# Kernel tuning notes

Measured on AMD Instinct MI355X. Metric: run time of the kernel, lower is better.

## Reference

```python
import jax, jax.numpy as jnp
import numpy as np


def setup_inputs() -> dict:
    key = jax.random.key(0)
    k1, k2 = jax.random.split(key)
    template = jax.random.normal(k1, (5, 8, 2), dtype=jnp.float32)        # (R, A, 2)
    projections = jax.random.normal(k2, (5000, 8, 2), dtype=jnp.float32)  # (V, K0, 2)
    return {"template": template, "projections": projections}


def _compute_bc(template, projections):
    # template: (R, A, 2); projections: (V, K0, 2)
    R, A = template.shape[:2]
    V, K0 = projections.shape[:2]
    K = K0 - 1  # number of 'other' (non-closest) neighbors

    # --- nearest-neighbor ordering of projected neighbors per template vertex ---
    diff = template[None, :, :, None, :] - projections[:, None, None, :, :]   # (V,R,A,K0,2)
    order = jnp.argsort(jnp.linalg.norm(diff, axis=-1), axis=-1)              # (V,R,A,K0)
    gathered = jnp.take_along_axis(projections[:, None, None, :, :], order[..., None], axis=3)  # (V,R,A,K0,2)
    closest = gathered[..., 0, :]   # (V,R,A,2)
    other = gathered[..., 1:, :]    # (V,R,A,K,2)

    # --- barycentric weights for every candidate (second, third) vertex pair ---
    # v0 == v1 in the original code (both other - closest)
    v0 = other - closest[..., None, :]          # (V,R,A,K,2)
    v2 = template[None] - closest               # (V,R,A,2)
    dot00 = jnp.einsum('vrani,vrani->vran', v0, v0)      # == dot11
    dot01 = jnp.einsum('vrani,vrami->vranm', v0, v0)
    dot02 = jnp.einsum('vrani,vrai->vran', v0, v2)       # == dot12

    eye = jnp.eye(K, dtype=bool)
    denom = dot00[..., :, None] * dot00[..., None, :] - dot01 * dot01   # (V,R,A,K,K)
    # original zeroes the diagonal then takes 1/0 = inf; we use a safe value and
    # explicitly invalidate the diagonal below (identical final output).
    inv = 1.0 / jnp.where(eye, 1.0, denom)
    w2 = (dot00[..., None, :] * dot02[..., :, None] - dot01 * dot02[..., None, :]) * inv
    w1 = (dot00[..., :, None] * dot02[..., None, :] - dot01 * dot02[..., :, None]) * inv
    w0 = 1.0 - w2 - w1
    weights = jnp.stack([w0, w2, w1], axis=-1)           # (V,R,A,K,K,3)

    invalid = (weights <= 0.0) | jnp.isnan(weights) | eye[:, :, None]
    weights = jnp.where(invalid, jnp.inf, weights)
    score = jnp.max(weights * weights, axis=-1)          # inf-norm of squared weights, (V,R,A,K,K)

    # --- Delaunay (empty-circumcircle) condition, dense over all (n, m, j) ---
    s_all = jnp.sum(gathered * gathered, axis=-1)        # x^2 + y^2, (V,R,A,K0)
    sc, so = s_all[..., 0], s_all[..., 1:]
    cx, cy = closest[..., 0], closest[..., 1]
    ox, oy = other[..., 0], other[..., 1]
    # rows of 4x4 incircle matrix: [closest, other[n], other[m], other[j]] with
    # columns [x, y, x^2+y^2, 1]; reduce rows by subtracting row 4 -> 3x3 det.
    ax = cx[..., None, None, None] - ox[..., None, None, :]   # (V,R,A,1,1,K)
    ay = cy[..., None, None, None] - oy[..., None, None, :]
    as_ = sc[..., None, None, None] - so[..., None, None, :]
    bx = ox[..., :, None, None] - ox[..., None, None, :]      # (V,R,A,K,1,K)
    by = oy[..., :, None, None] - oy[..., None, None, :]
    bs = so[..., :, None, None] - so[..., None, None, :]
    dx = ox[..., None, :, None] - ox[..., None, None, :]      # (V,R,A,1,K,K)
    dy = oy[..., None, :, None] - oy[..., None, None, :]
    ds = so[..., None, :, None] - so[..., None, None, :]
    det = ax * (by * ds - bs * dy) - ay * (bx * ds - bs * dx) + as_ * (bx * dy - by * dx)  # (V,R,A,K,K,K)
    j_is_tri = eye[:, None, :] | eye[None, :, :]              # exclude j == n or j == m
    ok = jnp.all((det <= 0.0) | j_is_tri, axis=-1)            # (V,R,A,K,K)
    score = jnp.where(ok, score, jnp.inf)

    # --- select best (second, third) pair per template vertex ---
    flat = score.reshape(V, R, A, K * K)
    idx = jnp.argmin(flat, axis=-1)                            # (V,R,A)
    row, col = idx // K, idx % K
    wf = weights.reshape(V, R, A, K * K, 3)
    w_sel = jnp.take_along_axis(wf, idx[..., None, None], axis=3)[..., 0, :]  # (V,R,A,3)
    zero_mask = jnp.any(jnp.isinf(w_sel), axis=-1, keepdims=True)
    w_sel = jnp.where(zero_mask, 0.0, w_sel)

    oh = order[..., 1:]                                        # (V,R,A,K)
    nbr_idx = jnp.take_along_axis(oh, jnp.stack([row, col], axis=-1), axis=-1)  # (V,R,A,2)
    indices = jnp.concatenate([order[..., :1], nbr_idx], axis=-1).astype(jnp.int32)  # (V,R,A,3)
    return w_sel, indices


def reference(template, projections):
    return _compute_bc(template, projections)
```

## Files before the change

### kernel.cpp

```cpp
#include <hip/hip_runtime.h>
#include <math.h>

#define R_DIM 5
#define A_DIM 8
#define K0    8
#define KK    7
#define NPAIR 21

#define PID(p, q) ((p) * 7 - (p) * ((p) + 1) / 2 + ((q) - (p) - 1))

__global__ __launch_bounds__(256) void bc_kernel(
    const float* __restrict__ tmpl,
    const float* __restrict__ proj,
    float* __restrict__ out,
    int ntask)
{
#pragma clang fp contract(off)
    const float INF = __builtin_inff();
    int tid = blockIdx.x * blockDim.x + threadIdx.x;
    if (tid >= ntask) return;
    int v  = tid / (R_DIM * A_DIM);
    int ra = tid - v * (R_DIM * A_DIM);

    float tx = tmpl[ra * 2 + 0];
    float ty = tmpl[ra * 2 + 1];

    const float4* pv4 = reinterpret_cast<const float4*>(proj + (size_t)v * (K0 * 2));
    float4 q0 = pv4[0], q1 = pv4[1], q2 = pv4[2], q3 = pv4[3];
    float px[K0] = {q0.x, q0.z, q1.x, q1.z, q2.x, q2.z, q3.x, q3.z};
    float py[K0] = {q0.y, q0.w, q1.y, q1.w, q2.y, q2.w, q3.y, q3.w};
    float ps[K0], pd[K0];
#pragma unroll
    for (int k = 0; k < K0; ++k) {
        ps[k] = px[k] * px[k] + py[k] * py[k];
        float dx = tx - px[k], dy = ty - py[k];
        pd[k] = sqrtf(dx * dx + dy * dy);
    }

    int rank[K0];
#pragma unroll
    for (int k = 0; k < K0; ++k) {
        int r = 0;
#pragma unroll
        for (int l = 0; l < K0; ++l)
            r += (pd[l] < pd[k] || (pd[l] == pd[k] && l < k)) ? 1 : 0;
        rank[k] = r;
    }

    float cx = 0.f, cy = 0.f, cs = 0.f; int cidx = 0;
#pragma unroll
    for (int k = 0; k < K0; ++k) {
        bool h = (rank[k] == 0);
        cx = h ? px[k] : cx;  cy = h ? py[k] : cy;
        cs = h ? ps[k] : cs;  cidx = h ? k : cidx;
    }

    float ox[KK], oy[KK], osq[KK]; int ork[KK], oid[KK];
#pragma unroll
    for (int n = 0; n < KK; ++n) {
        bool ge = (n >= cidx);
        ox[n]  = ge ? px[n + 1]   : px[n];
        oy[n]  = ge ? py[n + 1]   : py[n];
        osq[n] = ge ? ps[n + 1]   : ps[n];
        ork[n] = ge ? rank[n + 1] : rank[n];
        oid[n] = ge ? (n + 1)     : n;
    }

    float v2x = tx - cx, v2y = ty - cy;
    float vx[KK], vy[KK], d00[KK], d02[KK];
#pragma unroll
    for (int n = 0; n < KK; ++n) {
        vx[n] = ox[n] - cx;
        vy[n] = oy[n] - cy;
        d00[n] = vx[n] * vx[n] + vy[n] * vy[n];
        d02[n] = vx[n] * v2x + vy[n] * v2y;
    }

    float dmn[NPAIR], dmx[NPAIR];
#pragma unroll
    for (int i = 0; i < NPAIR; ++i) { dmn[i] = INF; dmx[i] = -INF; }

#pragma unroll
    for (int k = 0; k < KK; ++k) {
        float akx = cx - ox[k], aky = cy - oy[k], aks = cs - osq[k];
        float ex[KK], ey[KK], es[KK];
#pragma unroll
        for (int i = 0; i < KK; ++i) {
            if (i == k) continue;
            ex[i] = ox[i] - ox[k];
            ey[i] = oy[i] - oy[k];
            es[i] = osq[i] - osq[k];
        }
#pragma unroll
        for (int p = 0; p < KK - 1; ++p) {
#pragma unroll
            for (int q = p + 1; q < KK; ++q) {
                if (p == k || q == k) continue;
                const int pid = PID(p, q);
                float m1 = ey[p] * es[q] - es[p] * ey[q];
                float m2 = ex[p] * es[q] - es[p] * ex[q];
                float m3 = ex[p] * ey[q] - ey[p] * ex[q];
                float det = (akx * m1 - aky * m2) + aks * m3;
                dmn[pid] = fminf(dmn[pid], det);
                dmx[pid] = fmaxf(dmx[pid], det);
            }
        }
    }

    float bsc = INF; int brij = 0x7fffffff;
    float bw0 = 0.f, bw1 = 0.f, bw2 = 0.f;
    int bi = 0, bj = 0;

#pragma unroll
    for (int p = 0; p < KK - 1; ++p) {
#pragma unroll
        for (int q = p + 1; q < KK; ++q) {
            const int pid = PID(p, q);
            float d01 = vx[p] * vx[q] + vy[p] * vy[q];
            float den = d00[p] * d00[q] - d01 * d01;
            float inv = 1.0f / den;
            float u = (d00[q] * d02[p] - d01 * d02[q]) * inv;
            float w = (d00[p] * d02[q] - d01 * d02[p]) * inv;
            float w0a = (1.0f - u) - w;
            float w0b = (1.0f - w) - u;
            bool posuw = (u > 0.0f) && (w > 0.0f);
            bool okA = (dmx[pid] <= 0.0f);
            bool okB = (dmn[pid] >= 0.0f);
            float muw = fmaxf(u * u, w * w);
            float scA = fmaxf(w0a * w0a, muw);
            float scB = fmaxf(w0b * w0b, muw);
            int rpq = ork[p] * 8 + ork[q];
            int rqp = ork[q] * 8 + ork[p];

            bool vA = okA && posuw && (w0a > 0.0f) && (scA < INF);
            bool tA = vA && (scA < bsc || (scA == bsc && rpq < brij));
            bsc = tA ? scA : bsc;  brij = tA ? rpq : brij;
            bw0 = tA ? w0a : bw0;  bw2 = tA ? u : bw2;  bw1 = tA ? w : bw1;
            bi  = tA ? oid[p] : bi;  bj = tA ? oid[q] : bj;

            bool vB = okB && posuw && (w0b > 0.0f) && (scB < INF);
            bool tB = vB && (scB < bsc || (scB == bsc && rqp < brij));
            bsc = tB ? scB : bsc;  brij = tB ? rqp : brij;
            bw0 = tB ? w0b : bw0;  bw2 = tB ? w : bw2;  bw1 = tB ? u : bw1;
            bi  = tB ? oid[q] : bi;  bj = tB ? oid[p] : bj;
        }
    }

    int sec = 0;
#pragma unroll
    for (int n = 0; n < KK; ++n) sec = (ork[n] == 1) ? oid[n] : sec;
    bool found = (bsc < INF);
    float o0 = found ? bw0 : 0.0f;
    float o1 = found ? bw2 : 0.0f;
    float o2 = found ? bw1 : 0.0f;
    int j1 = found ? bi : sec;
    int j2 = found ? bj : sec;

    size_t ob = (size_t)tid * 3;
    out[ob + 0] = o0;
    out[ob + 1] = o1;
    out[ob + 2] = o2;
    size_t off = (size_t)ntask * 3;
    out[off + ob + 0] = (float)cidx;
    out[off + ob + 1] = (float)j1;
    out[off + ob + 2] = (float)j2;
}

extern "C" void kernel_launch(void* const* d_in, const int* in_sizes, int n_in,
                              void* d_out, int out_size, void* d_ws, size_t ws_size,
                              hipStream_t stream) {
    const float* tmpl = (const float*)d_in[0];
    const float* proj = (const float*)d_in[1];
    float* out = (float*)d_out;

    int V = in_sizes[1] / (K0 * 2);
    int ntask = V * R_DIM * A_DIM;
    int threads = 256;
    int blocks = (ntask + threads - 1) / threads;
    bc_kernel<<<blocks, threads, 0, stream>>>(tmpl, proj, out, ntask);
}
```

Baseline: 81.17 us.

## Split candidate pairs across four wavefronts per task with shared-memory argmin

Each task is now processed by four wavefronts. Each wavefront evaluates a subset of the 21 candidate pairs, and the results are reduced through shared memory using a packed score/rank key. The determinant test is recomputed per pair rather than accumulated into 21-entry min/max arrays, which cuts register pressure. In exchange, the setup work (sorting, neighbour selection) is repeated four times, a block barrier is added, and there is no bounds check when ntask is not a multiple of 64.

```diff
diff --git a/kernel.cpp b/kernel.cpp
--- a/kernel.cpp
+++ b/kernel.cpp
@@ -5,11 +5,51 @@
 #define A_DIM 8
 #define K0    8
 #define KK    7
-#define NPAIR 21
-
-#define PID(p, q) ((p) * 7 - (p) * ((p) + 1) / 2 + ((q) - (p) - 1))
-
-__global__ __launch_bounds__(256) void bc_kernel(
+#define TPB   256
+#define TASKS_PER_BLOCK 64
+
+#define DO_PAIR(p, q) do {                                                    \
+    float d01 = vx[(p)]*vx[(q)] + vy[(p)]*vy[(q)];                            \
+    float den = d00[(p)]*d00[(q)] - d01*d01;                                  \
+    float inv = 1.0f/den;                                                     \
+    float u   = (d00[(q)]*d02[(p)] - d01*d02[(q)]) * inv;                     \
+    float w   = (d00[(p)]*d02[(q)] - d01*d02[(p)]) * inv;                     \
+    float w0a = (1.0f - u) - w;                                               \
+    float w0b = (1.0f - w) - u;                                               \
+    float dmnP = INF, dmxP = -INF;                                            \
+    _Pragma("unroll")                                                         \
+    for (int j = 0; j < KK; ++j) {                                            \
+        if (j == (p) || j == (q)) continue;          \
+        float bx = ox[(p)]-ox[j], by = oy[(p)]-oy[j], bs = osq[(p)]-osq[j];   \
+        float dx = ox[(q)]-ox[j], dy = oy[(q)]-oy[j], ds = osq[(q)]-osq[j];   \
+        float m1 = by*ds - bs*dy;                                             \
+        float m2 = bx*ds - bs*dx;                                             \
+        float m3 = bx*dy - by*dx;                                             \
+        float det = (ajx[j]*m1 - ajy[j]*m2) + ajs[j]*m3;                      \
+        dmnP = fminf(dmnP, det);                                              \
+        dmxP = fmaxf(dmxP, det);                                              \
+    }                                                                         \
+    bool posuw = (u > 0.0f) && (w > 0.0f);                                    \
+    bool okA = (dmxP <= 0.0f);                                                \
+    bool okB = (dmnP >= 0.0f);                                                \
+    float muw = fmaxf(u*u, w*w);                                              \
+    float scA = fmaxf(w0a*w0a, muw);                                          \
+    float scB = fmaxf(w0b*w0b, muw);                                          \
+    int rpq = ork[(p)]*8 + ork[(q)];                                          \
+    int rqp = ork[(q)]*8 + ork[(p)];                                          \
+    bool vA = okA && posuw && (w0a > 0.0f) && (scA < INF);                    \
+    bool tA = vA && (scA < bsc || (scA == bsc && rpq < brij));                \
+    bsc = tA ? scA : bsc;  brij = tA ? rpq : brij;                            \
+    bw0 = tA ? w0a : bw0;  bw2 = tA ? u : bw2;  bw1 = tA ? w : bw1;           \
+    bi  = tA ? oid[(p)] : bi;  bj = tA ? oid[(q)] : bj;                       \
+    bool vB = okB && posuw && (w0b > 0.0f) && (scB < INF);                    \
+    bool tB = vB && (scB < bsc || (scB == bsc && rqp < brij));                \
+    bsc = tB ? scB : bsc;  brij = tB ? rqp : brij;                            \
+    bw0 = tB ? w0b : bw0;  bw2 = tB ? w : bw2;  bw1 = tB ? u : bw1;           \
+    bi  = tB ? oid[(q)] : bi;  bj = tB ? oid[(p)] : bj;                       \
+} while (0)
+
+__global__ __launch_bounds__(TPB) void bc_kernel(
     const float* __restrict__ tmpl,
     const float* __restrict__ proj,
     float* __restrict__ out,
@@ -17,10 +57,19 @@
 {
 #pragma clang fp contract(off)
     const float INF = __builtin_inff();
-    int tid = blockIdx.x * blockDim.x + threadIdx.x;
-    if (tid >= ntask) return;
-    int v  = tid / (R_DIM * A_DIM);
-    int ra = tid - v * (R_DIM * A_DIM);
+
+    __shared__ unsigned long long skey[4][TASKS_PER_BLOCK];
+    __shared__ float sw0[4][TASKS_PER_BLOCK];
+    __shared__ float sw2[4][TASKS_PER_BLOCK];
+    __shared__ float sw1[4][TASKS_PER_BLOCK];
+    __shared__ int   sbi[4][TASKS_PER_BLOCK];
+    __shared__ int   sbj[4][TASKS_PER_BLOCK];
+
+    int lane = threadIdx.x & 63;
+    int wid  = threadIdx.x >> 6;
+    int task = blockIdx.x * TASKS_PER_BLOCK + lane;
+    int v  = task / (R_DIM * A_DIM);
+    int ra = task - v * (R_DIM * A_DIM);
 
     float tx = tmpl[ra * 2 + 0];
     float ty = tmpl[ra * 2 + 1];
@@ -68,102 +117,73 @@
 
     float v2x = tx - cx, v2y = ty - cy;
     float vx[KK], vy[KK], d00[KK], d02[KK];
+    float ajx[KK], ajy[KK], ajs[KK];
 #pragma unroll
     for (int n = 0; n < KK; ++n) {
         vx[n] = ox[n] - cx;
         vy[n] = oy[n] - cy;
         d00[n] = vx[n] * vx[n] + vy[n] * vy[n];
         d02[n] = vx[n] * v2x + vy[n] * v2y;
-    }
-
-    float dmn[NPAIR], dmx[NPAIR];
-#pragma unroll
-    for (int i = 0; i < NPAIR; ++i) { dmn[i] = INF; dmx[i] = -INF; }
-
-#pragma unroll
-    for (int k = 0; k < KK; ++k) {
-        float akx = cx - ox[k], aky = cy - oy[k], aks = cs - osq[k];
-        float ex[KK], ey[KK], es[KK];
-#pragma unroll
-        for (int i = 0; i < KK; ++i) {
-            if (i == k) continue;
-            ex[i] = ox[i] - ox[k];
-            ey[i] = oy[i] - oy[k];
-            es[i] = osq[i] - osq[k];
-        }
-#pragma unroll
-        for (int p = 0; p < KK - 1; ++p) {
-#pragma unroll
-            for (int q = p + 1; q < KK; ++q) {
-                if (p == k || q == k) continue;
-                const int pid = PID(p, q);
-                float m1 = ey[p] * es[q] - es[p] * ey[q];
-                float m2 = ex[p] * es[q] - es[p] * ex[q];
-                float m3 = ex[p] * ey[q] - ey[p] * ex[q];
-                float det = (akx * m1 - aky * m2) + aks * m3;
-                dmn[pid] = fminf(dmn[pid], det);
-                dmx[pid] = fmaxf(dmx[pid], det);
-            }
-        }
+        ajx[n] = cx - ox[n];
+        ajy[n] = cy - oy[n];
+        ajs[n] = cs - osq[n];
     }
 
     float bsc = INF; int brij = 0x7fffffff;
     float bw0 = 0.f, bw1 = 0.f, bw2 = 0.f;
     int bi = 0, bj = 0;
 
-#pragma unroll
-    for (int p = 0; p < KK - 1; ++p) {
-#pragma unroll
-        for (int q = p + 1; q < KK; ++q) {
-            const int pid = PID(p, q);
-            float d01 = vx[p] * vx[q] + vy[p] * vy[q];
-            float den = d00[p] * d00[q] - d01 * d01;
-            float inv = 1.0f / den;
-            float u = (d00[q] * d02[p] - d01 * d02[q]) * inv;
-            float w = (d00[p] * d02[q] - d01 * d02[p]) * inv;
-            float w0a = (1.0f - u) - w;
-            float w0b = (1.0f - w) - u;
-            bool posuw = (u > 0.0f) && (w > 0.0f);
-            bool okA = (dmx[pid] <= 0.0f);
-            bool okB = (dmn[pid] >= 0.0f);
-            float muw = fmaxf(u * u, w * w);
-            float scA = fmaxf(w0a * w0a, muw);
-            float scB = fmaxf(w0b * w0b, muw);
-            int rpq = ork[p] * 8 + ork[q];
-            int rqp = ork[q] * 8 + ork[p];
-
-            bool vA = okA && posuw && (w0a > 0.0f) && (scA < INF);
-            bool tA = vA && (scA < bsc || (scA == bsc && rpq < brij));
-            bsc = tA ? scA : bsc;  brij = tA ? rpq : brij;
-            bw0 = tA ? w0a : bw0;  bw2 = tA ? u : bw2;  bw1 = tA ? w : bw1;
-            bi  = tA ? oid[p] : bi;  bj = tA ? oid[q] : bj;
-
-            bool vB = okB && posuw && (w0b > 0.0f) && (scB < INF);
-            bool tB = vB && (scB < bsc || (scB == bsc && rqp < brij));
-            bsc = tB ? scB : bsc;  brij = tB ? rqp : brij;
-            bw0 = tB ? w0b : bw0;  bw2 = tB ? w : bw2;  bw1 = tB ? u : bw1;
-            bi  = tB ? oid[q] : bi;  bj = tB ? oid[p] : bj;
-        }
-    }
-
-    int sec = 0;
-#pragma unroll
-    for (int n = 0; n < KK; ++n) sec = (ork[n] == 1) ? oid[n] : sec;
-    bool found = (bsc < INF);
-    float o0 = found ? bw0 : 0.0f;
-    float o1 = found ? bw2 : 0.0f;
-    float o2 = found ? bw1 : 0.0f;
-    int j1 = found ? bi : sec;
-    int j2 = found ? bj : sec;
-
-    size_t ob = (size_t)tid * 3;
-    out[ob + 0] = o0;
-    out[ob + 1] = o1;
-    out[ob + 2] = o2;
-    size_t off = (size_t)ntask * 3;
-    out[off + ob + 0] = (float)cidx;
-    out[off + ob + 1] = (float)j1;
-    out[off + ob + 2] = (float)j2;
+    if (wid == 0) {
+        DO_PAIR(0,1); DO_PAIR(0,2); DO_PAIR(0,3);
+        DO_PAIR(0,4); DO_PAIR(0,5); DO_PAIR(0,6);
+    } else if (wid == 1) {
+        DO_PAIR(1,2); DO_PAIR(1,3); DO_PAIR(1,4);
+        DO_PAIR(1,5); DO_PAIR(1,6);
+    } else if (wid == 2) {
+        DO_PAIR(2,3); DO_PAIR(2,4); DO_PAIR(2,5);
+        DO_PAIR(2,6); DO_PAIR(5,6);
+    } else {
+        DO_PAIR(3,4); DO_PAIR(3,5); DO_PAIR(3,6);
+        DO_PAIR(4,5); DO_PAIR(4,6);
+    }
+
+    unsigned long long key =
+        ((unsigned long long)__float_as_uint(bsc) << 32) | (unsigned int)brij;
+    skey[wid][lane] = key;
+    sw0[wid][lane] = bw0;
+    sw2[wid][lane] = bw2;
+    sw1[wid][lane] = bw1;
+    sbi[wid][lane] = bi;
+    sbj[wid][lane] = bj;
+    __syncthreads();
+
+    if (wid == 0) {
+        unsigned long long mk = skey[0][lane]; int ws = 0;
+        unsigned long long k;
+        k = skey[1][lane]; if (k < mk) { mk = k; ws = 1; }
+        k = skey[2][lane]; if (k < mk) { mk = k; ws = 2; }
+        k = skey[3][lane]; if (k < mk) { mk = k; ws = 3; }
+        bool found = ((unsigned int)(mk >> 32)) != 0x7f800000u;
+
+        int sec = 0;
+#pragma unroll
+        for (int n = 0; n < KK; ++n) sec = (ork[n] == 1) ? oid[n] : sec;
+
+        float o0 = found ? sw0[ws][lane] : 0.0f;
+        float o1 = found ? sw2[ws][lane] : 0.0f;
+        float o2 = found ? sw1[ws][lane] : 0.0f;
+        int j1 = found ? sbi[ws][lane] : sec;
+        int j2 = found ? sbj[ws][lane] : sec;
+
+        size_t ob = (size_t)task * 3;
+        out[ob + 0] = o0;
+        out[ob + 1] = o1;
+        out[ob + 2] = o2;
+        size_t off = (size_t)ntask * 3;
+        out[off + ob + 0] = (float)cidx;
+        out[off + ob + 1] = (float)j1;
+        out[off + ob + 2] = (float)j2;
+    }
 }
 
 extern "C" void kernel_launch(void* const* d_in, const int* in_sizes, int n_in,
@@ -175,7 +195,6 @@
 
     int V = in_sizes[1] / (K0 * 2);
     int ntask = V * R_DIM * A_DIM;
-    int threads = 256;
-    int blocks = (ntask + threads - 1) / threads;
-    bc_kernel<<<blocks, threads, 0, stream>>>(tmpl, proj, out, ntask);
+    int blocks = (ntask + TASKS_PER_BLOCK - 1) / TASKS_PER_BLOCK;
+    bc_kernel<<<blocks, TPB, 0, stream>>>(tmpl, proj, out, ntask);
 }
```

New measurement: 84.62 us. +4.3%, slower.
